# Kernel tuning notes

Hardware: AMD Instinct MI355X
Metric: run time of the kernel (lower is better)

## Reference

```python
import jax, jax.numpy as jnp
import numpy as np

H = 64          # rnn_hidden_dim
HYP = 64        # api_hyper_dim
N_AG = 8
N_EN = 8
N_AL = 7
E_FEAT = 9
A_FEAT = 10
OWN_FEAT = 16
N_ACT = 14


def setup_inputs() -> dict:
    key = jax.random.key(0)
    ks = jax.random.split(key, 24)
    bs = 4096
    inp = {
        "own_feats": jax.random.normal(ks[0], (bs * N_AG, OWN_FEAT), jnp.float32),
        "enemy_feats": jax.random.normal(ks[1], (bs * N_AG * N_EN, E_FEAT), jnp.float32),
        "ally_feats": jax.random.normal(ks[2], (bs * N_AG * N_AL, A_FEAT), jnp.float32),
        "hidden_state": jax.random.normal(ks[3], (bs * N_AG, H), jnp.float32),
        "agent_indices": jax.random.randint(ks[4], (bs * N_AG,), 0, N_AG),
        "last_action_indices": jax.random.randint(ks[5], (bs * N_AG,), 0, N_ACT),
        "bs": bs,
    }
    s = 0.05
    inp.update({
        "fc1_own_w": jax.random.normal(ks[6], (OWN_FEAT, H), jnp.float32) * s,
        "fc1_own_b": jnp.zeros((H,), jnp.float32),
        "agent_id_emb": jax.random.normal(ks[7], (N_AG, H), jnp.float32) * s,
        "action_id_emb": jax.random.normal(ks[8], (N_ACT, H), jnp.float32) * s,
        "he_w1": jax.random.normal(ks[9], (E_FEAT, HYP), jnp.float32) * s,
        "he_b1": jnp.zeros((HYP,), jnp.float32),
        "he_w2": jax.random.normal(ks[10], (HYP, (E_FEAT + 1) * H + 1), jnp.float32) * s,
        "he_b2": jnp.zeros(((E_FEAT + 1) * H + 1,), jnp.float32),
        "ha_w1": jax.random.normal(ks[11], (A_FEAT, HYP), jnp.float32) * s,
        "ha_b1": jnp.zeros((HYP,), jnp.float32),
        "ha_w2": jax.random.normal(ks[12], (HYP, A_FEAT * H), jnp.float32) * s,
        "ha_b2": jnp.zeros((A_FEAT * H,), jnp.float32),
        "gru_w_ih": jax.random.normal(ks[13], (3 * H, H), jnp.float32) * s,
        "gru_w_hh": jax.random.normal(ks[14], (3 * H, H), jnp.float32) * s,
        "gru_b_ih": jnp.zeros((3 * H,), jnp.float32),
        "gru_b_hh": jnp.zeros((3 * H,), jnp.float32),
        "fc2_w": jax.random.normal(ks[15], (H, 6), jnp.float32) * s,
        "fc2_b": jnp.zeros((6,), jnp.float32),
    })
    return inp


def reference(own_feats, enemy_feats, ally_feats, hidden_state,
              fc1_own_w, fc1_own_b, agent_id_emb, action_id_emb,
              he_w1, he_b1, he_w2, he_b2, ha_w1, ha_b1, ha_w2, ha_b2,
              gru_w_ih, gru_w_hh, gru_b_ih, gru_b_hh, fc2_w, fc2_b,
              agent_indices, last_action_indices, bs):
    # own embedding + id/action embeddings  [bs*n_ag, H]
    emb_own = own_feats @ fc1_own_w + fc1_own_b
    emb_own = emb_own + agent_id_emb[agent_indices] + action_id_emb[last_action_indices]

    # enemy hypernet: [bs*n_ag*n_en, (E_FEAT+1)*H + 1]
    hyper_e = jax.nn.relu(enemy_feats @ he_w1 + he_b1) @ he_w2 + he_b2
    fc1_w_e = hyper_e[:, :-(H + 1)].reshape(-1, E_FEAT, H)
    emb_en = jnp.einsum('ne,neh->nh', enemy_feats, fc1_w_e)
    emb_en = emb_en.reshape(bs * N_AG, N_EN, H).sum(axis=1)

    # ally hypernet (non-MMM): [bs*n_ag*n_al, A_FEAT*H]
    hyper_a = jax.nn.relu(ally_feats @ ha_w1 + ha_b1) @ ha_w2 + ha_b2
    fc1_w_a = hyper_a.reshape(-1, A_FEAT, H)
    emb_al = jnp.einsum('na,nah->nh', ally_feats, fc1_w_a)
    emb_al = emb_al.reshape(bs * N_AG, N_AL, H).sum(axis=1)

    x = jax.nn.relu(emb_own + emb_en + emb_al)

    # torch GRUCell
    h_in = hidden_state.reshape(-1, H)
    gi = x @ gru_w_ih.T + gru_b_ih
    gh = h_in @ gru_w_hh.T + gru_b_hh
    i_r, i_z, i_n = jnp.split(gi, 3, axis=-1)
    h_r, h_z, h_n = jnp.split(gh, 3, axis=-1)
    r = jax.nn.sigmoid(i_r + h_r)
    z = jax.nn.sigmoid(i_z + h_z)
    n = jnp.tanh(i_n + r * h_n)
    hh = (1.0 - z) * n + z * h_in

    q_normal = (hh @ fc2_w + fc2_b).reshape(bs, N_AG, 6)

    # attack head from enemy hypernet tail
    fc2_w_attack = hyper_e[:, -(H + 1):-1].reshape(bs * N_AG, N_EN, H)
    fc2_b_attack = hyper_e[:, -1].reshape(bs * N_AG, N_EN)
    q_attack = (jnp.einsum('nh,neh->ne', hh, fc2_w_attack) + fc2_b_attack).reshape(bs, N_AG, N_EN)

    q = jnp.concatenate([q_normal, q_attack], axis=-1)
    return q.reshape(bs, N_AG, -1), hh.reshape(bs, N_AG, H)
```

## Files before the change

### kernel.cpp

```cpp
#include <hip/hip_runtime.h>
#include <hip/hip_bf16.h>

typedef short short8 __attribute__((ext_vector_type(8)));
typedef float f32x4 __attribute__((ext_vector_type(4)));

#define HD 64
#define N_EN 8
#define N_AL 7
#define E_FEAT 9
#define A_FEAT 10
#define OWN_FEAT 16
#define N_ACT 14
#define EW2 641
#define AW2 640

#define KSE 20
#define KSA 21
#define KSG 5
#define KSU 3

#define BE_OFF 0
#define BE_CNT (KSE*4*64*8)
#define BA_OFF (BE_OFF+BE_CNT)
#define BA_CNT (KSA*4*64*8)
#define BG_OFF (BA_OFF+BA_CNT)
#define BG_CNT (KSG*16*64*8)
#define BU_OFF (BG_OFF+BG_CNT)
#define BU_CNT (KSU*5*64*8)
#define WS_SHORTS (BU_OFF+BU_CNT)

#define P_STRIDE 676
#define LDS_AG 0
#define LDS_GATES 8192
#define LDS_AU 17024
#define LDS_U 0
#define LDS_BYTES 21632

__device__ __forceinline__ ushort f2u(float x) {
    __hip_bfloat16 b = __float2bfloat16(x);
    ushort u; __builtin_memcpy(&u, &b, 2); return u;
}
__device__ __forceinline__ float u2f(uint u) {
    union { uint x; float f; } c; c.x = u << 16; return c.f;
}
__device__ __forceinline__ uint pk2(float a, float b) {
    return (uint)f2u(a) | ((uint)f2u(b) << 16);
}
__device__ __forceinline__ float sigm(float x) { return 1.f / (1.f + __expf(-x)); }
__device__ __forceinline__ short8 lda(const char* base, int row, int strideB, int s, int g) {
    const char* p = base + row * strideB + s * 64 + g * 8;
    union { short8 v; uint2 q[2]; } u;
    u.q[0] = *(const uint2*)p;
    u.q[1] = *(const uint2*)(p + 32);
    return u.v;
}

__global__ __launch_bounds__(256) void prep_kernel(
    const float* __restrict__ he_w2, const float* __restrict__ he_b2,
    const float* __restrict__ ha_w2, const float* __restrict__ ha_b2,
    const float* __restrict__ fc1_own_w, const float* __restrict__ fc1_own_b,
    const float* __restrict__ agent_id_emb, const float* __restrict__ action_id_emb,
    const float* __restrict__ gru_w_ih, const float* __restrict__ gru_w_hh,
    const float* __restrict__ gru_b_ih, const float* __restrict__ gru_b_hh,
    const float* __restrict__ fc2_w, const float* __restrict__ fc2_b,
    ushort* __restrict__ ws)
{
    const int GE = KSE * 4, GA = KSA * 4, GG = KSG * 16, GU = KSU * 5;
    const int total = (GE + GA + GG + GU) * 64;
    int idx = blockIdx.x * 256 + threadIdx.x;
    if (idx >= total) return;
    int grp = idx >> 6, lane = idx & 63;
    int g = lane >> 4, col16 = lane & 15;
    int table, s, t, slot;
    if (grp < GE)           { table = 0; int q = grp;            s = q / 4;  t = q % 4;  slot = q * 64 + lane; }
    else if (grp < GE + GA) { table = 1; int q = grp - GE;       s = q / 4;  t = q % 4;  slot = q * 64 + lane; }
    else if (grp < GE + GA + GG) { table = 2; int q = grp - GE - GA; s = q / 16; t = q % 16; slot = q * 64 + lane; }
    else                    { table = 3; int q = grp - GE - GA - GG; s = q / 5; t = q % 5; slot = q * 64 + lane; }
    const int j = t * 16 + col16;
    ushort out[8];
    #pragma unroll
    for (int e = 0; e < 8; ++e) {
        int kk = 32 * s + 4 * g + (e & 3) + 16 * (e >> 2);
        float v = 0.f;
        if (table == 0) {
            if (kk < 576)      { int f = kk >> 6, k = kk & 63; v = he_w2[k * EW2 + f * HD + j]; }
            else if (kk < 585) { int f = kk - 576; v = he_b2[f * HD + j]; }
            else if (kk < 601) { int f = kk - 585; v = fc1_own_w[f * HD + j]; }
            else if (kk == 601){ v = fc1_own_b[j]; }
            else if (kk < 610) { int a = kk - 602; v = agent_id_emb[a * HD + j]; }
            else if (kk < 624) { int a = kk - 610; v = action_id_emb[a * HD + j]; }
        } else if (table == 1) {
            if (kk < 640)      { int f = kk >> 6, k = kk & 63; v = ha_w2[k * AW2 + f * HD + j]; }
            else if (kk < 650) { int f = kk - 640; v = ha_b2[f * HD + j]; }
        } else if (table == 2) {
            int gb = j >> 6, c = j & 63;
            if (gb <= 1) {
                int jj = gb * 64 + c;
                if (kk < 64)        v = gru_w_ih[jj * HD + kk];
                else if (kk < 128)  v = gru_w_hh[jj * HD + kk - 64];
                else if (kk == 128) v = gru_b_ih[jj] + gru_b_hh[jj];
            } else if (gb == 2) {
                int jj = 128 + c;
                if (kk < 64)        v = gru_w_ih[jj * HD + kk];
                else if (kk == 128) v = gru_b_ih[jj];
            } else {
                int jj = 128 + c;
                if (kk >= 64 && kk < 128) v = gru_w_hh[jj * HD + kk - 64];
                else if (kk == 128)       v = gru_b_hh[jj];
            }
        } else {
            if (j < 64) {
                if (kk < 64)       v = he_w2[j * EW2 + 576 + kk];
                else if (kk == 64) v = he_w2[j * EW2 + 640];
            } else if (j < 70) {
                int o = j - 64;
                if (kk < 64)       v = fc2_w[kk * 6 + o];
                else if (kk == 64) v = fc2_b[o];
            } else if (j == 70) {
                if (kk < 64)       v = he_b2[576 + kk];
                else if (kk == 64) v = he_b2[640];
            }
        }
        out[e] = f2u(v);
    }
    ushort* dst = ws + ((table == 0) ? BE_OFF : (table == 1) ? BA_OFF : (table == 2) ? BG_OFF : BU_OFF);
    *(short8*)(dst + slot * 8) = *(short8*)out;
}

__global__ __launch_bounds__(256, 4) void agent_kernel(
    const float* __restrict__ own_feats,
    const float* __restrict__ enemy_feats,
    const float* __restrict__ ally_feats,
    const float* __restrict__ hidden_state,
    const int*  __restrict__ agent_idx,
    const int*  __restrict__ last_act_idx,
    const float* __restrict__ he_w1, const float* __restrict__ he_b1,
    const float* __restrict__ ha_w1, const float* __restrict__ ha_b1,
    const ushort* __restrict__ ws,
    float* __restrict__ out_q, float* __restrict__ out_hh)
{
    __shared__ __align__(16) char smem[LDS_BYTES];
    const int tid  = threadIdx.x;
    const int lane = tid & 63;
    const int wv   = tid >> 6;
    const int n0   = blockIdx.x * 16;
    const int arow = lane & 15;
    const int g    = lane >> 4;
    ushort* P = (ushort*)smem;

    {
        float w1[E_FEAT];
        #pragma unroll
        for (int f = 0; f < E_FEAT; ++f) w1[f] = he_w1[f * HD + lane];
        const float b1 = he_b1[lane];
        #pragma unroll
        for (int rr = 0; rr < 4; ++rr) {
            const int row = wv * 4 + rr, n = n0 + row;
            const float* efb = enemy_feats + (size_t)n * (N_EN * E_FEAT);
            float pf[E_FEAT];
            #pragma unroll
            for (int f = 0; f < E_FEAT; ++f) pf[f] = 0.f;
            #pragma unroll
            for (int e = 0; e < N_EN; ++e) {
                float ef[E_FEAT];
                #pragma unroll
                for (int f = 0; f < E_FEAT; ++f) ef[f] = efb[e * E_FEAT + f];
                float acc = b1;
                #pragma unroll
                for (int f = 0; f < E_FEAT; ++f) acc += ef[f] * w1[f];
                const float r = fmaxf(acc, 0.f);
                #pragma unroll
                for (int f = 0; f < E_FEAT; ++f) pf[f] += r * ef[f];
            }
            ushort* Pr = P + row * P_STRIDE;
            #pragma unroll
            for (int f = 0; f < E_FEAT; ++f) Pr[f * HD + lane] = f2u(pf[f]);
            if (lane < E_FEAT) {
                float sv = 0.f;
                #pragma unroll
                for (int e = 0; e < N_EN; ++e) sv += efb[e * E_FEAT + lane];
                Pr[576 + lane] = f2u(sv);
            }
            if (lane == 20) Pr[601] = 0x3F80;
            if (lane < OWN_FEAT) Pr[585 + lane] = f2u(own_feats[(size_t)n * OWN_FEAT + lane]);
            const int ai = agent_idx[n], la = last_act_idx[n];
            if (lane < 8)      Pr[602 + lane] = (lane == ai) ? 0x3F80 : 0;
            if (lane < N_ACT)  Pr[610 + lane] = (lane == la) ? 0x3F80 : 0;
            if (lane < 16)     Pr[624 + lane] = 0;
        }
    }
    __syncthreads();

    f32x4 accE = {0.f, 0.f, 0.f, 0.f};
    __builtin_amdgcn_s_setprio(1);
    #pragma unroll 5
    for (int s = 0; s < KSE; ++s) {
        short8 b = *(const short8*)(ws + BE_OFF + ((size_t)(s * 4 + wv) * 64 + lane) * 8);
        short8 a = lda(smem, arow, P_STRIDE * 2, s, g);
        accE = __builtin_amdgcn_mfma_f32_16x16x32_bf16(a, b, accE, 0, 0, 0);
    }
    __builtin_amdgcn_s_setprio(0);
    __syncthreads();

    {
        float w1[A_FEAT];
        #pragma unroll
        for (int f = 0; f < A_FEAT; ++f) w1[f] = ha_w1[f * HD + lane];
        const float b1 = ha_b1[lane];
        #pragma unroll
        for (int rr = 0; rr < 4; ++rr) {
            const int row = wv * 4 + rr, n = n0 + row;
            const float* afb = ally_feats + (size_t)n * (N_AL * A_FEAT);
            float pf[A_FEAT];
            #pragma unroll
            for (int f = 0; f < A_FEAT; ++f) pf[f] = 0.f;
            #pragma unroll
            for (int e = 0; e < N_AL; ++e) {
                float af[A_FEAT];
                #pragma unroll
                for (int f = 0; f < A_FEAT; ++f) af[f] = afb[e * A_FEAT + f];
                float acc = b1;
                #pragma unroll
                for (int f = 0; f < A_FEAT; ++f) acc += af[f] * w1[f];
                const float r = fmaxf(acc, 0.f);
                #pragma unroll
                for (int f = 0; f < A_FEAT; ++f) pf[f] += r * af[f];
            }
            ushort* Pr = P + row * P_STRIDE;
            #pragma unroll
            for (int f = 0; f < A_FEAT; ++f) Pr[f * HD + lane] = f2u(pf[f]);
            if (lane < A_FEAT) {
                float sv = 0.f;
                #pragma unroll
                for (int e = 0; e < N_AL; ++e) sv += afb[e * A_FEAT + lane];
                Pr[640 + lane] = f2u(sv);
            }
            if (lane < 22) Pr[650 + lane] = 0;
        }
    }
    __syncthreads();

    __builtin_amdgcn_s_setprio(1);
    #pragma unroll 7
    for (int s = 0; s < KSA; ++s) {
        short8 b = *(const short8*)(ws + BA_OFF + ((size_t)(s * 4 + wv) * 64 + lane) * 8);
        short8 a = lda(smem, arow, P_STRIDE * 2, s, g);
        accE = __builtin_amdgcn_mfma_f32_16x16x32_bf16(a, b, accE, 0, 0, 0);
    }
    __builtin_amdgcn_s_setprio(0);
    __syncthreads();

    #pragma unroll
    for (int j = 0; j < 4; ++j) {
        const int m = g * 4 + j;
        *(ushort*)(smem + LDS_AG + m * 328 + (wv * 16 + arow) * 2) = f2u(fmaxf(accE[j], 0.f));
    }
    {
        const int row = tid >> 4, c4 = (tid & 15) * 4;
        float4 h4 = *(const float4*)(hidden_state + (size_t)(n0 + row) * HD + c4);
        char* p = smem + LDS_AG + row * 328 + (64 + c4) * 2;
        *(uint*)p       = pk2(h4.x, h4.y);
        *(uint*)(p + 4) = pk2(h4.z, h4.w);
        if (tid < 16) *(ushort*)(smem + LDS_AG + tid * 328 + 128 * 2) = 0x3F80;
        for (int i = tid; i < 16 * 31; i += 256) {
            int r2 = i / 31, c = 129 + i % 31;
            *(ushort*)(smem + LDS_AG + r2 * 328 + c * 2) = 0;
        }
    }
    __syncthreads();

    {
        f32x4 accG[4] = {{0.f,0.f,0.f,0.f},{0.f,0.f,0.f,0.f},{0.f,0.f,0.f,0.f},{0.f,0.f,0.f,0.f}};
        __builtin_amdgcn_s_setprio(1);
        #pragma unroll
        for (int s = 0; s < KSG; ++s) {
            short8 a = lda(smem + LDS_AG, arow, 328, s, g);
            #pragma unroll
            for (int tt = 0; tt < 4; ++tt) {
                const int t = wv * 4 + tt;
                short8 b = *(const short8*)(ws + BG_OFF + ((size_t)(s * 16 + t) * 64 + lane) * 8);
                accG[tt] = __builtin_amdgcn_mfma_f32_16x16x32_bf16(a, b, accG[tt], 0, 0, 0);
            }
        }
        __builtin_amdgcn_s_setprio(0);
        #pragma unroll
        for (int tt = 0; tt < 4; ++tt)
            #pragma unroll
            for (int j = 0; j < 4; ++j) {
                const int m = g * 4 + j, jc = (wv * 4 + tt) * 16 + arow;
                *(ushort*)(smem + LDS_GATES + m * 520 + jc * 2) = f2u(accG[tt][j]);
            }
    }
    __syncthreads();

    {
        const int row = tid >> 4, c4 = (tid & 15) * 4;
        const char* gb = smem + LDS_GATES + row * 520;
        uint2 rv = *(const uint2*)(gb + c4 * 2);
        uint2 zv = *(const uint2*)(gb + 128 + c4 * 2);
        uint2 iv = *(const uint2*)(gb + 256 + c4 * 2);
        uint2 nv = *(const uint2*)(gb + 384 + c4 * 2);
        float4 h4 = *(const float4*)(hidden_state + (size_t)(n0 + row) * HD + c4);
        float hr[4] = {u2f(rv.x & 0xffffu), u2f(rv.x >> 16), u2f(rv.y & 0xffffu), u2f(rv.y >> 16)};
        float hz[4] = {u2f(zv.x & 0xffffu), u2f(zv.x >> 16), u2f(zv.y & 0xffffu), u2f(zv.y >> 16)};
        float hi[4] = {u2f(iv.x & 0xffffu), u2f(iv.x >> 16), u2f(iv.y & 0xffffu), u2f(iv.y >> 16)};
        float hn[4] = {u2f(nv.x & 0xffffu), u2f(nv.x >> 16), u2f(nv.y & 0xffffu), u2f(nv.y >> 16)};
        float hcur[4] = {h4.x, h4.y, h4.z, h4.w};
        float hh[4];
        #pragma unroll
        for (int cc = 0; cc < 4; ++cc) {
            const float r = sigm(hr[cc]);
            const float z = sigm(hz[cc]);
            const float nng = tanhf(hi[cc] + r * hn[cc]);
            hh[cc] = (1.f - z) * nng + z * hcur[cc];
        }
        *(float4*)(out_hh + (size_t)(n0 + row) * HD + c4) = make_float4(hh[0], hh[1], hh[2], hh[3]);
        char* p = smem + LDS_AU + row * 200 + c4 * 2;
        *(uint*)p       = pk2(hh[0], hh[1]);
        *(uint*)(p + 4) = pk2(hh[2], hh[3]);
        if (tid < 16) *(ushort*)(smem + LDS_AU + tid * 200 + 64 * 2) = 0x3F80;
        for (int i = tid; i < 16 * 31; i += 256) {
            int r2 = i / 31, c = 65 + i % 31;
            *(ushort*)(smem + LDS_AU + r2 * 200 + c * 2) = 0;
        }
    }
    __syncthreads();

    {
        f32x4 accU = {0.f, 0.f, 0.f, 0.f};
        f32x4 accQ = {0.f, 0.f, 0.f, 0.f};
        __builtin_amdgcn_s_setprio(1);
        #pragma unroll
        for (int s = 0; s < KSU; ++s) {
            short8 a = lda(smem + LDS_AU, arow, 200, s, g);
            short8 b = *(const short8*)(ws + BU_OFF + ((size_t)(s * 5 + wv) * 64 + lane) * 8);
            accU = __builtin_amdgcn_mfma_f32_16x16x32_bf16(a, b, accU, 0, 0, 0);
            if (wv == 0) {
                short8 b2 = *(const short8*)(ws + BU_OFF + ((size_t)(s * 5 + 4) * 64 + lane) * 8);
                accQ = __builtin_amdgcn_mfma_f32_16x16x32_bf16(a, b2, accQ, 0, 0, 0);
            }
        }
        __builtin_amdgcn_s_setprio(0);
        float* uld = (float*)(smem + LDS_U);
        #pragma unroll
        for (int j = 0; j < 4; ++j) {
            const int m = g * 4 + j;
            uld[m * 66 + wv * 16 + arow] = accU[j];
        }
        if (wv == 0) {
            #pragma unroll
            for (int j = 0; j < 4; ++j) {
                const int m = g * 4 + j;
                if (arow < 6)       out_q[(size_t)(n0 + m) * N_ACT + arow] = accQ[j];
                else if (arow == 6) uld[m * 66 + 64] = accQ[j];
            }
        }
    }
    __syncthreads();

    {
        float w1[E_FEAT];
        #pragma unroll
        for (int f = 0; f < E_FEAT; ++f) w1[f] = he_w1[f * HD + lane];
        const float b1 = he_b1[lane];
        const float* uld = (const float*)(smem + LDS_U);
        #pragma unroll
        for (int rr = 0; rr < 4; ++rr) {
            const int row = wv * 4 + rr, n = n0 + row;
            const float uk = uld[row * 66 + lane];
            const float ct = uld[row * 66 + 64];
            const float* efb = enemy_feats + (size_t)n * (N_EN * E_FEAT);
            float p[N_EN];
            #pragma unroll
            for (int e = 0; e < N_EN; ++e) {
                float acc = b1;
                #pragma unroll
                for (int f = 0; f < E_FEAT; ++f) acc += efb[e * E_FEAT + f] * w1[f];
                p[e] = fmaxf(acc, 0.f) * uk;
            }
            #pragma unroll
            for (int o = 1; o < 64; o <<= 1) {
                #pragma unroll
                for (int e = 0; e < N_EN; ++e) p[e] += __shfl_xor(p[e], o);
            }
            if (lane < N_EN) {
                float pv = p[0];
                #pragma unroll
                for (int e = 1; e < N_EN; ++e) if (lane == e) pv = p[e];
                out_q[(size_t)n * N_ACT + 6 + lane] = pv + ct;
            }
        }
    }
}

extern "C" void kernel_launch(void* const* d_in, const int* in_sizes, int n_in,
                              void* d_out, int out_size, void* d_ws, size_t ws_size,
                              hipStream_t stream) {
    const float* own_feats    = (const float*)d_in[0];
    const float* enemy_feats  = (const float*)d_in[1];
    const float* ally_feats   = (const float*)d_in[2];
    const float* hidden_state = (const float*)d_in[3];
    const int*  agent_idx     = (const int*)d_in[4];
    const int*  last_act      = (const int*)d_in[5];
    const float* fc1_own_w = (const float*)d_in[7];
    const float* fc1_own_b = (const float*)d_in[8];
    const float* agent_id_emb  = (const float*)d_in[9];
    const float* action_id_emb = (const float*)d_in[10];
    const float* he_w1 = (const float*)d_in[11];
    const float* he_b1 = (const float*)d_in[12];
    const float* he_w2 = (const float*)d_in[13];
    const float* he_b2 = (const float*)d_in[14];
    const float* ha_w1 = (const float*)d_in[15];
    const float* ha_b1 = (const float*)d_in[16];
    const float* ha_w2 = (const float*)d_in[17];
    const float* ha_b2 = (const float*)d_in[18];
    const float* gru_w_ih = (const float*)d_in[19];
    const float* gru_w_hh = (const float*)d_in[20];
    const float* gru_b_ih = (const float*)d_in[21];
    const float* gru_b_hh = (const float*)d_in[22];
    const float* fc2_w = (const float*)d_in[23];
    const float* fc2_b = (const float*)d_in[24];

    const int R = in_sizes[0] / OWN_FEAT;
    ushort* ws = (ushort*)d_ws;
    float* out_q  = (float*)d_out;
    float* out_hh = out_q + (size_t)R * N_ACT;

    prep_kernel<<<65, 256, 0, stream>>>(
        he_w2, he_b2, ha_w2, ha_b2, fc1_own_w, fc1_own_b,
        agent_id_emb, action_id_emb, gru_w_ih, gru_w_hh, gru_b_ih, gru_b_hh,
        fc2_w, fc2_b, ws);

    agent_kernel<<<R / 16, 256, 0, stream>>>(
        own_feats, enemy_feats, ally_feats, hidden_state, agent_idx, last_act,
        he_w1, he_b1, ha_w1, ha_b1, ws, out_q, out_hh);
}
```

Baseline: 91.59 us.

## Trim MFMA K-steps, move biases to fp32 epilogue, XOR-swizzle LDS rows

The ally bias-sum rows are folded into the enemy table's padding, so the ally GEMM drops from 21 to 20 K-steps. The GRU and output GEMMs each lose one K-step because their bias rows now come from a small fp32 bias buffer added in the epilogue, which also removes the LDS padding and ones-column writes. The P activation buffer now uses a 640-wide row with an XOR swizzle to avoid LDS bank conflicts, and all LDS offsets shrink. In exchange it adds extra global bias loads in the epilogues and more index arithmetic for the swizzle.

After: 90.64 us, median of 2. No clear change (-1.0%).

```diff
diff --git a/kernel.cpp b/kernel.cpp
--- a/kernel.cpp
+++ b/kernel.cpp
@@ -14,27 +14,21 @@
 #define EW2 641
 #define AW2 640
 
-#define KSE 20
-#define KSA 21
-#define KSG 5
-#define KSU 3
+#define PW 640
+#define LDS_BYTES 20480
+#define AG_OFF 0
+#define AG_STR 264
+#define GATES_OFF 4352
+#define GT_STR 520
+#define AU_OFF 12672
+#define AU_STR 136
+#define U_OFF 0
 
 #define BE_OFF 0
-#define BE_CNT (KSE*4*64*8)
-#define BA_OFF (BE_OFF+BE_CNT)
-#define BA_CNT (KSA*4*64*8)
-#define BG_OFF (BA_OFF+BA_CNT)
-#define BG_CNT (KSG*16*64*8)
-#define BU_OFF (BG_OFF+BG_CNT)
-#define BU_CNT (KSU*5*64*8)
-#define WS_SHORTS (BU_OFF+BU_CNT)
-
-#define P_STRIDE 676
-#define LDS_AG 0
-#define LDS_GATES 8192
-#define LDS_AU 17024
-#define LDS_U 0
-#define LDS_BYTES 21632
+#define BA_OFF 40960
+#define BG_OFF 81920
+#define BU_OFF 114688
+#define WS_US 119808
 
 __device__ __forceinline__ ushort f2u(float x) {
     __hip_bfloat16 b = __float2bfloat16(x);
@@ -47,7 +41,17 @@
     return (uint)f2u(a) | ((uint)f2u(b) << 16);
 }
 __device__ __forceinline__ float sigm(float x) { return 1.f / (1.f + __expf(-x)); }
-__device__ __forceinline__ short8 lda(const char* base, int row, int strideB, int s, int g) {
+
+__device__ __forceinline__ short8 lda_swz(const ushort* P_us, int row, int s, int g) {
+    const int mm = (row & 7) << 3;
+    const int o = s * 32 + g * 4;
+    const ushort* pr = P_us + row * PW;
+    union { short8 v; uint2 q[2]; } u;
+    u.q[0] = *(const uint2*)(pr + (o ^ mm));
+    u.q[1] = *(const uint2*)(pr + ((o + 16) ^ mm));
+    return u.v;
+}
+__device__ __forceinline__ short8 lda_lin(const char* base, int row, int strideB, int s, int g) {
     const char* p = base + row * strideB + s * 64 + g * 8;
     union { short8 v; uint2 q[2]; } u;
     u.q[0] = *(const uint2*)p;
@@ -63,68 +67,61 @@
     const float* __restrict__ gru_w_ih, const float* __restrict__ gru_w_hh,
     const float* __restrict__ gru_b_ih, const float* __restrict__ gru_b_hh,
     const float* __restrict__ fc2_w, const float* __restrict__ fc2_b,
-    ushort* __restrict__ ws)
+    ushort* __restrict__ ws, float* __restrict__ fbias)
 {
-    const int GE = KSE * 4, GA = KSA * 4, GG = KSG * 16, GU = KSU * 5;
-    const int total = (GE + GA + GG + GU) * 64;
+    const int GE = 80, GA = 80, GG = 64, GU = 10;
+    const int TT = (GE + GA + GG + GU) * 64;
     int idx = blockIdx.x * 256 + threadIdx.x;
-    if (idx >= total) return;
-    int grp = idx >> 6, lane = idx & 63;
-    int g = lane >> 4, col16 = lane & 15;
-    int table, s, t, slot;
-    if (grp < GE)           { table = 0; int q = grp;            s = q / 4;  t = q % 4;  slot = q * 64 + lane; }
-    else if (grp < GE + GA) { table = 1; int q = grp - GE;       s = q / 4;  t = q % 4;  slot = q * 64 + lane; }
-    else if (grp < GE + GA + GG) { table = 2; int q = grp - GE - GA; s = q / 16; t = q % 16; slot = q * 64 + lane; }
-    else                    { table = 3; int q = grp - GE - GA - GG; s = q / 5; t = q % 5; slot = q * 64 + lane; }
-    const int j = t * 16 + col16;
-    ushort out[8];
-    #pragma unroll
-    for (int e = 0; e < 8; ++e) {
-        int kk = 32 * s + 4 * g + (e & 3) + 16 * (e >> 2);
-        float v = 0.f;
-        if (table == 0) {
-            if (kk < 576)      { int f = kk >> 6, k = kk & 63; v = he_w2[k * EW2 + f * HD + j]; }
-            else if (kk < 585) { int f = kk - 576; v = he_b2[f * HD + j]; }
-            else if (kk < 601) { int f = kk - 585; v = fc1_own_w[f * HD + j]; }
-            else if (kk == 601){ v = fc1_own_b[j]; }
-            else if (kk < 610) { int a = kk - 602; v = agent_id_emb[a * HD + j]; }
-            else if (kk < 624) { int a = kk - 610; v = action_id_emb[a * HD + j]; }
-        } else if (table == 1) {
-            if (kk < 640)      { int f = kk >> 6, k = kk & 63; v = ha_w2[k * AW2 + f * HD + j]; }
-            else if (kk < 650) { int f = kk - 640; v = ha_b2[f * HD + j]; }
-        } else if (table == 2) {
-            int gb = j >> 6, c = j & 63;
-            if (gb <= 1) {
-                int jj = gb * 64 + c;
-                if (kk < 64)        v = gru_w_ih[jj * HD + kk];
-                else if (kk < 128)  v = gru_w_hh[jj * HD + kk - 64];
-                else if (kk == 128) v = gru_b_ih[jj] + gru_b_hh[jj];
-            } else if (gb == 2) {
-                int jj = 128 + c;
-                if (kk < 64)        v = gru_w_ih[jj * HD + kk];
-                else if (kk == 128) v = gru_b_ih[jj];
+    if (idx < TT) {
+        int grp = idx >> 6, lane = idx & 63;
+        int g = lane >> 4, col16 = lane & 15;
+        int table, s, t, slot;
+        if (grp < GE)                { table = 0; int q = grp;                s = q / 4;  t = q % 4;  slot = q * 64 + lane; }
+        else if (grp < GE + GA)      { table = 1; int q = grp - GE;           s = q / 4;  t = q % 4;  slot = q * 64 + lane; }
+        else if (grp < GE + GA + GG) { table = 2; int q = grp - GE - GA;      s = q / 16; t = q % 16; slot = q * 64 + lane; }
+        else                         { table = 3; int q = grp - GE - GA - GG; s = q / 5;  t = q % 5;  slot = q * 64 + lane; }
+        const int j = t * 16 + col16;
+        ushort out[8];
+        #pragma unroll
+        for (int e = 0; e < 8; ++e) {
+            int kk = 32 * s + 4 * g + (e & 3) + 16 * (e >> 2);
+            float v = 0.f;
+            if (table == 0) {
+                if (kk < 576)       v = he_w2[(kk & 63) * EW2 + (kk >> 6) * HD + j];
+                else if (kk < 585)  v = he_b2[(kk - 576) * HD + j];
+                else if (kk < 601)  v = fc1_own_w[(kk - 585) * HD + j];
+                else if (kk == 601) v = fc1_own_b[j];
+                else if (kk < 610)  v = agent_id_emb[(kk - 602) * HD + j];
+                else if (kk < 624)  v = action_id_emb[(kk - 610) * HD + j];
+                else if (kk < 634)  v = ha_b2[(kk - 624) * HD + j];
+            } else if (table == 1) {
+                v = ha_w2[(kk & 63) * AW2 + (kk >> 6) * HD + j];
+            } else if (table == 2) {
+                int gb2 = j >> 6, c = j & 63;
+                int jj = (gb2 == 0) ? c : (gb2 == 1) ? 64 + c : 128 + c;
+                if (gb2 <= 1)      v = (kk < 64) ? gru_w_ih[jj * HD + kk] : gru_w_hh[jj * HD + kk - 64];
+                else if (gb2 == 2) v = (kk < 64) ? gru_w_ih[jj * HD + kk] : 0.f;
+                else               v = (kk >= 64) ? gru_w_hh[jj * HD + kk - 64] : 0.f;
             } else {
-                int jj = 128 + c;
-                if (kk >= 64 && kk < 128) v = gru_w_hh[jj * HD + kk - 64];
-                else if (kk == 128)       v = gru_b_hh[jj];
-            }
-        } else {
-            if (j < 64) {
-                if (kk < 64)       v = he_w2[j * EW2 + 576 + kk];
-                else if (kk == 64) v = he_w2[j * EW2 + 640];
-            } else if (j < 70) {
-                int o = j - 64;
-                if (kk < 64)       v = fc2_w[kk * 6 + o];
-                else if (kk == 64) v = fc2_b[o];
-            } else if (j == 70) {
-                if (kk < 64)       v = he_b2[576 + kk];
-                else if (kk == 64) v = he_b2[640];
-            }
-        }
-        out[e] = f2u(v);
-    }
-    ushort* dst = ws + ((table == 0) ? BE_OFF : (table == 1) ? BA_OFF : (table == 2) ? BG_OFF : BU_OFF);
-    *(short8*)(dst + slot * 8) = *(short8*)out;
+                if (kk < 64) {
+                    if (j < 64)       v = he_w2[j * EW2 + 576 + kk];
+                    else if (j < 70)  v = fc2_w[kk * 6 + (j - 64)];
+                    else if (j == 70) v = he_b2[576 + kk];
+                }
+            }
+            out[e] = f2u(v);
+        }
+        ushort* dst = ws + ((table == 0) ? BE_OFF : (table == 1) ? BA_OFF : (table == 2) ? BG_OFF : BU_OFF);
+        *(short8*)(dst + (size_t)slot * 8) = *(short8*)out;
+    } else {
+        int b = idx - TT;
+        if (b < 128)       fbias[b] = gru_b_ih[b] + gru_b_hh[b];
+        else if (b < 192)  fbias[b] = gru_b_ih[b];
+        else if (b < 256)  fbias[b] = gru_b_hh[b - 64];
+        else if (b < 320)  fbias[b] = he_w2[(size_t)(b - 256) * EW2 + 640];
+        else if (b < 326)  fbias[b] = fc2_b[b - 320];
+        else if (b == 326) fbias[326] = he_b2[640];
+    }
 }
 
 __global__ __launch_bounds__(256, 4) void agent_kernel(
@@ -136,7 +133,7 @@
     const int*  __restrict__ last_act_idx,
     const float* __restrict__ he_w1, const float* __restrict__ he_b1,
     const float* __restrict__ ha_w1, const float* __restrict__ ha_b1,
-    const ushort* __restrict__ ws,
+    const ushort* __restrict__ ws, const float* __restrict__ fbias,
     float* __restrict__ out_q, float* __restrict__ out_hh)
 {
     __shared__ __align__(16) char smem[LDS_BYTES];
@@ -156,6 +153,7 @@
         #pragma unroll
         for (int rr = 0; rr < 4; ++rr) {
             const int row = wv * 4 + rr, n = n0 + row;
+            const int mm = (row & 7) << 3;
             const float* efb = enemy_feats + (size_t)n * (N_EN * E_FEAT);
             float pf[E_FEAT];
             #pragma unroll
@@ -172,21 +170,28 @@
                 #pragma unroll
                 for (int f = 0; f < E_FEAT; ++f) pf[f] += r * ef[f];
             }
-            ushort* Pr = P + row * P_STRIDE;
-            #pragma unroll
-            for (int f = 0; f < E_FEAT; ++f) Pr[f * HD + lane] = f2u(pf[f]);
+            ushort* Pr = P + row * PW;
+            #pragma unroll
+            for (int f = 0; f < E_FEAT; ++f) Pr[(f * HD + lane) ^ mm] = f2u(pf[f]);
             if (lane < E_FEAT) {
                 float sv = 0.f;
                 #pragma unroll
                 for (int e = 0; e < N_EN; ++e) sv += efb[e * E_FEAT + lane];
-                Pr[576 + lane] = f2u(sv);
-            }
-            if (lane == 20) Pr[601] = 0x3F80;
-            if (lane < OWN_FEAT) Pr[585 + lane] = f2u(own_feats[(size_t)n * OWN_FEAT + lane]);
+                Pr[(576 + lane) ^ mm] = f2u(sv);
+            }
+            if (lane < OWN_FEAT) Pr[(585 + lane) ^ mm] = f2u(own_feats[(size_t)n * OWN_FEAT + lane]);
+            if (lane == 20) Pr[601 ^ mm] = 0x3F80;
             const int ai = agent_idx[n], la = last_act_idx[n];
-            if (lane < 8)      Pr[602 + lane] = (lane == ai) ? 0x3F80 : 0;
-            if (lane < N_ACT)  Pr[610 + lane] = (lane == la) ? 0x3F80 : 0;
-            if (lane < 16)     Pr[624 + lane] = 0;
+            if (lane < 8)      Pr[(602 + lane) ^ mm] = (lane == ai) ? (ushort)0x3F80 : (ushort)0;
+            if (lane < N_ACT)  Pr[(610 + lane) ^ mm] = (lane == la) ? (ushort)0x3F80 : (ushort)0;
+            if (lane < A_FEAT) {
+                const float* afb = ally_feats + (size_t)n * (N_AL * A_FEAT);
+                float sv = 0.f;
+                #pragma unroll
+                for (int e = 0; e < N_AL; ++e) sv += afb[e * A_FEAT + lane];
+                Pr[(624 + lane) ^ mm] = f2u(sv);
+            }
+            if (lane < 6) Pr[(634 + lane) ^ mm] = 0;
         }
     }
     __syncthreads();
@@ -194,9 +199,9 @@
     f32x4 accE = {0.f, 0.f, 0.f, 0.f};
     __builtin_amdgcn_s_setprio(1);
     #pragma unroll 5
-    for (int s = 0; s < KSE; ++s) {
+    for (int s = 0; s < 20; ++s) {
         short8 b = *(const short8*)(ws + BE_OFF + ((size_t)(s * 4 + wv) * 64 + lane) * 8);
-        short8 a = lda(smem, arow, P_STRIDE * 2, s, g);
+        short8 a = lda_swz(P, arow, s, g);
         accE = __builtin_amdgcn_mfma_f32_16x16x32_bf16(a, b, accE, 0, 0, 0);
     }
     __builtin_amdgcn_s_setprio(0);
@@ -210,6 +215,7 @@
         #pragma unroll
         for (int rr = 0; rr < 4; ++rr) {
             const int row = wv * 4 + rr, n = n0 + row;
+            const int mm = (row & 7) << 3;
             const float* afb = ally_feats + (size_t)n * (N_AL * A_FEAT);
             float pf[A_FEAT];
             #pragma unroll
@@ -226,25 +232,18 @@
                 #pragma unroll
                 for (int f = 0; f < A_FEAT; ++f) pf[f] += r * af[f];
             }
-            ushort* Pr = P + row * P_STRIDE;
-            #pragma unroll
-            for (int f = 0; f < A_FEAT; ++f) Pr[f * HD + lane] = f2u(pf[f]);
-            if (lane < A_FEAT) {
-                float sv = 0.f;
-                #pragma unroll
-                for (int e = 0; e < N_AL; ++e) sv += afb[e * A_FEAT + lane];
-                Pr[640 + lane] = f2u(sv);
-            }
-            if (lane < 22) Pr[650 + lane] = 0;
+            ushort* Pr = P + row * PW;
+            #pragma unroll
+            for (int f = 0; f < A_FEAT; ++f) Pr[(f * HD + lane) ^ mm] = f2u(pf[f]);
         }
     }
     __syncthreads();
 
     __builtin_amdgcn_s_setprio(1);
-    #pragma unroll 7
-    for (int s = 0; s < KSA; ++s) {
+    #pragma unroll 5
+    for (int s = 0; s < 20; ++s) {
         short8 b = *(const short8*)(ws + BA_OFF + ((size_t)(s * 4 + wv) * 64 + lane) * 8);
-        short8 a = lda(smem, arow, P_STRIDE * 2, s, g);
+        short8 a = lda_swz(P, arow, s, g);
         accE = __builtin_amdgcn_mfma_f32_16x16x32_bf16(a, b, accE, 0, 0, 0);
     }
     __builtin_amdgcn_s_setprio(0);
@@ -253,19 +252,14 @@
     #pragma unroll
     for (int j = 0; j < 4; ++j) {
         const int m = g * 4 + j;
-        *(ushort*)(smem + LDS_AG + m * 328 + (wv * 16 + arow) * 2) = f2u(fmaxf(accE[j], 0.f));
+        *(ushort*)(smem + AG_OFF + m * AG_STR + (wv * 16 + arow) * 2) = f2u(fmaxf(accE[j], 0.f));
     }
     {
         const int row = tid >> 4, c4 = (tid & 15) * 4;
         float4 h4 = *(const float4*)(hidden_state + (size_t)(n0 + row) * HD + c4);
-        char* p = smem + LDS_AG + row * 328 + (64 + c4) * 2;
+        char* p = smem + AG_OFF + row * AG_STR + (64 + c4) * 2;
         *(uint*)p       = pk2(h4.x, h4.y);
         *(uint*)(p + 4) = pk2(h4.z, h4.w);
-        if (tid < 16) *(ushort*)(smem + LDS_AG + tid * 328 + 128 * 2) = 0x3F80;
-        for (int i = tid; i < 16 * 31; i += 256) {
-            int r2 = i / 31, c = 129 + i % 31;
-            *(ushort*)(smem + LDS_AG + r2 * 328 + c * 2) = 0;
-        }
     }
     __syncthreads();
 
@@ -273,8 +267,8 @@
         f32x4 accG[4] = {{0.f,0.f,0.f,0.f},{0.f,0.f,0.f,0.f},{0.f,0.f,0.f,0.f},{0.f,0.f,0.f,0.f}};
         __builtin_amdgcn_s_setprio(1);
         #pragma unroll
-        for (int s = 0; s < KSG; ++s) {
-            short8 a = lda(smem + LDS_AG, arow, 328, s, g);
+        for (int s = 0; s < 4; ++s) {
+            short8 a = lda_lin(smem + AG_OFF, arow, AG_STR, s, g);
             #pragma unroll
             for (int tt = 0; tt < 4; ++tt) {
                 const int t = wv * 4 + tt;
@@ -284,18 +278,21 @@
         }
         __builtin_amdgcn_s_setprio(0);
         #pragma unroll
-        for (int tt = 0; tt < 4; ++tt)
+        for (int tt = 0; tt < 4; ++tt) {
+            const int jc = (wv * 4 + tt) * 16 + arow;
+            const float bt = fbias[jc];
             #pragma unroll
             for (int j = 0; j < 4; ++j) {
-                const int m = g * 4 + j, jc = (wv * 4 + tt) * 16 + arow;
-                *(ushort*)(smem + LDS_GATES + m * 520 + jc * 2) = f2u(accG[tt][j]);
-            }
+                const int m = g * 4 + j;
+                *(ushort*)(smem + GATES_OFF + m * GT_STR + jc * 2) = f2u(accG[tt][j] + bt);
+            }
+        }
     }
     __syncthreads();
 
     {
         const int row = tid >> 4, c4 = (tid & 15) * 4;
-        const char* gb = smem + LDS_GATES + row * 520;
+        const char* gb = smem + GATES_OFF + row * GT_STR;
         uint2 rv = *(const uint2*)(gb + c4 * 2);
         uint2 zv = *(const uint2*)(gb + 128 + c4 * 2);
         uint2 iv = *(const uint2*)(gb + 256 + c4 * 2);
@@ -315,14 +312,9 @@
             hh[cc] = (1.f - z) * nng + z * hcur[cc];
         }
         *(float4*)(out_hh + (size_t)(n0 + row) * HD + c4) = make_float4(hh[0], hh[1], hh[2], hh[3]);
-        char* p = smem + LDS_AU + row * 200 + c4 * 2;
+        char* p = smem + AU_OFF + row * AU_STR + c4 * 2;
         *(uint*)p       = pk2(hh[0], hh[1]);
         *(uint*)(p + 4) = pk2(hh[2], hh[3]);
-        if (tid < 16) *(ushort*)(smem + LDS_AU + tid * 200 + 64 * 2) = 0x3F80;
-        for (int i = tid; i < 16 * 31; i += 256) {
-            int r2 = i / 31, c = 65 + i % 31;
-            *(ushort*)(smem + LDS_AU + r2 * 200 + c * 2) = 0;
-        }
     }
     __syncthreads();
 
@@ -331,8 +323,8 @@
         f32x4 accQ = {0.f, 0.f, 0.f, 0.f};
         __builtin_amdgcn_s_setprio(1);
         #pragma unroll
-        for (int s = 0; s < KSU; ++s) {
-            short8 a = lda(smem + LDS_AU, arow, 200, s, g);
+        for (int s = 0; s < 2; ++s) {
+            short8 a = lda_lin(smem + AU_OFF, arow, AU_STR, s, g);
             short8 b = *(const short8*)(ws + BU_OFF + ((size_t)(s * 5 + wv) * 64 + lane) * 8);
             accU = __builtin_amdgcn_mfma_f32_16x16x32_bf16(a, b, accU, 0, 0, 0);
             if (wv == 0) {
@@ -341,18 +333,19 @@
             }
         }
         __builtin_amdgcn_s_setprio(0);
-        float* uld = (float*)(smem + LDS_U);
+        float* uld = (float*)(smem + U_OFF);
+        const float ub = fbias[256 + wv * 16 + arow];
         #pragma unroll
         for (int j = 0; j < 4; ++j) {
             const int m = g * 4 + j;
-            uld[m * 66 + wv * 16 + arow] = accU[j];
+            uld[m * 66 + wv * 16 + arow] = accU[j] + ub;
         }
         if (wv == 0) {
             #pragma unroll
             for (int j = 0; j < 4; ++j) {
                 const int m = g * 4 + j;
-                if (arow < 6)       out_q[(size_t)(n0 + m) * N_ACT + arow] = accQ[j];
-                else if (arow == 6) uld[m * 66 + 64] = accQ[j];
+                if (arow < 6)       out_q[(size_t)(n0 + m) * N_ACT + arow] = accQ[j] + fbias[320 + arow];
+                else if (arow == 6) uld[m * 66 + 64] = accQ[j] + fbias[326];
             }
         }
     }
@@ -363,7 +356,7 @@
         #pragma unroll
         for (int f = 0; f < E_FEAT; ++f) w1[f] = he_w1[f * HD + lane];
         const float b1 = he_b1[lane];
-        const float* uld = (const float*)(smem + LDS_U);
+        const float* uld = (const float*)(smem + U_OFF);
         #pragma unroll
         for (int rr = 0; rr < 4; ++rr) {
             const int row = wv * 4 + rr, n = n0 + row;
@@ -423,15 +416,16 @@
 
     const int R = in_sizes[0] / OWN_FEAT;
     ushort* ws = (ushort*)d_ws;
+    float* fbias = (float*)(ws + WS_US);
     float* out_q  = (float*)d_out;
     float* out_hh = out_q + (size_t)R * N_ACT;
 
-    prep_kernel<<<65, 256, 0, stream>>>(
+    prep_kernel<<<60, 256, 0, stream>>>(
         he_w2, he_b2, ha_w2, ha_b2, fc1_own_w, fc1_own_b,
         agent_id_emb, action_id_emb, gru_w_ih, gru_w_hh, gru_b_ih, gru_b_hh,
-        fc2_w, fc2_b, ws);
+        fc2_w, fc2_b, ws, fbias);
 
     agent_kernel<<<R / 16, 256, 0, stream>>>(
         own_feats, enemy_feats, ally_feats, hidden_state, agent_idx, last_act,
-        he_w1, he_b1, ha_w1, ha_b1, ws, out_q, out_hh);
-}
+        he_w1, he_b1, ha_w1, ha_b1, ws, fbias, out_q, out_hh);
+}
```
